# Optimization experiments

Measured on AMD Instinct MI355X. Metric: run time of the kernel, lower is better.

Reference implementation:

```python
import jax, jax.numpy as jnp
import numpy as np

N_NODES = 50000
N_EDGES = 800000
F_IN = 128
F_HID = 128
N_CLS = 1
E_TR = 100000
E_TE = 20000


def setup_inputs() -> dict:
    key = jax.random.key(0)
    ks = jax.random.split(key, 16)
    inp = {
        'x': jax.random.normal(ks[0], (N_NODES, F_IN), dtype=jnp.float32),
        'edge_index': jax.random.randint(ks[1], (2, N_EDGES), 0, N_NODES, dtype=jnp.int32),
        'pos_edges_train': jax.random.randint(ks[2], (2, E_TR), 0, N_NODES, dtype=jnp.int32),
        'neg_edges_train': jax.random.randint(ks[3], (2, E_TR), 0, N_NODES, dtype=jnp.int32),
        'pos_edges_test': jax.random.randint(ks[4], (2, E_TE), 0, N_NODES, dtype=jnp.int32),
        'neg_edges_test': jax.random.randint(ks[5], (2, E_TE), 0, N_NODES, dtype=jnp.int32),
    }
    s = 0.05
    inp['W0'] = jax.random.normal(ks[6], (F_IN, F_HID), dtype=jnp.float32) * s
    inp['b0'] = jnp.zeros((F_HID,), dtype=jnp.float32)
    inp['W1'] = jax.random.normal(ks[7], (F_HID, F_HID), dtype=jnp.float32) * s
    inp['b1'] = jnp.zeros((F_HID,), dtype=jnp.float32)
    inp['W2'] = jax.random.normal(ks[8], (F_HID, F_HID), dtype=jnp.float32) * s
    inp['b2'] = jnp.zeros((F_HID,), dtype=jnp.float32)
    inp['W3'] = jax.random.normal(ks[9], (F_HID, F_HID), dtype=jnp.float32) * s
    inp['b3'] = jnp.zeros((F_HID,), dtype=jnp.float32)
    inp['Wl1'] = jax.random.normal(ks[10], (2 * F_HID, F_HID), dtype=jnp.float32) * s
    inp['bl1'] = jnp.zeros((F_HID,), dtype=jnp.float32)
    inp['Wl2'] = jax.random.normal(ks[11], (F_HID, N_CLS), dtype=jnp.float32) * s
    inp['bl2'] = jnp.zeros((N_CLS,), dtype=jnp.float32)
    return inp


def _gcn_conv(h, W, b, src, dst, dis):
    # PyG GCNConv: out = D^{-1/2}(A+I)D^{-1/2} (h W) + b, with self loops folded in analytically
    hw = h @ W                                           # [N, F]
    msg = hw[src] * dis[src][:, None]                    # [E, F]
    agg = jax.ops.segment_sum(msg, dst, num_segments=N_NODES)
    return agg * dis[:, None] + hw * (dis ** 2)[:, None] + b


def _edge_feats(x, e):
    return jnp.concatenate([x[e[0]], x[e[1]]], axis=1)


def reference(x, edge_index, pos_edges_train, neg_edges_train, pos_edges_test, neg_edges_test,
              W0, b0, W1, b1, W2, b2, W3, b3, Wl1, bl1, Wl2, bl2):
    src, dst = edge_index[0], edge_index[1]
    # degree with self loop (+1), symmetric normalization
    deg = jax.ops.segment_sum(jnp.ones((src.shape[0],), jnp.float32), dst, num_segments=N_NODES) + 1.0
    dis = deg ** -0.5

    h = jax.nn.relu(_gcn_conv(x, W0, b0, src, dst, dis))
    h = jax.nn.relu(_gcn_conv(h, W1, b1, src, dst, dis))
    h = jax.nn.relu(_gcn_conv(h, W2, b2, src, dst, dis))
    h = _gcn_conv(h, W3, b3, src, dst, dis)

    x_train = jnp.concatenate([_edge_feats(h, pos_edges_train), _edge_feats(h, neg_edges_train)], axis=0)
    x_test = jnp.concatenate([_edge_feats(h, pos_edges_test), _edge_feats(h, neg_edges_test)], axis=0)
    n_train = x_train.shape[0]
    z = jnp.concatenate([x_train, x_test], axis=0)
    z = jax.nn.relu(z @ Wl1 + bl1)
    z = (z @ Wl2 + bl2).squeeze(1)
    return (z[:n_train], z[n_train:])
```

## Files before the change

### kernel.cpp

```cpp
#include <hip/hip_runtime.h>
#include <math.h>

#define NN 50000
#define NE 800000
#define FD 128
#define SCAN_B 196


__global__ __launch_bounds__(256) void k_zero_int(int* __restrict__ p, int n) {
    int i = blockIdx.x * 256 + threadIdx.x;
    if (i < n) p[i] = 0;
}

__global__ __launch_bounds__(256) void k_count(const int* __restrict__ dst, int* __restrict__ deg) {
    int e = blockIdx.x * 256 + threadIdx.x;
    if (e < NE) atomicAdd(&deg[dst[e]], 1);
}


__global__ __launch_bounds__(256) void k_scan1(const int* __restrict__ deg,
                                               int* __restrict__ partial,
                                               int* __restrict__ bsum,
                                               float* __restrict__ dis) {
    __shared__ int wsum[4];
    const int t = threadIdx.x, lane = t & 63, wid = t >> 6;
    const int i = blockIdx.x * 256 + t;
    int v = (i < NN) ? deg[i] : 0;
    int sc = v;
#pragma unroll
    for (int d = 1; d < 64; d <<= 1) {
        int o = __shfl_up(sc, d, 64);
        if (lane >= d) sc += o;
    }
    if (lane == 63) wsum[wid] = sc;
    __syncthreads();
    int pre = 0;
    for (int w = 0; w < wid; ++w) pre += wsum[w];
    if (i < NN) {
        partial[i] = pre + sc - v;
        dis[i] = (float)(1.0 / sqrt((double)(v + 1)));
    }
    if (t == 255) bsum[blockIdx.x] = pre + sc;
}


__global__ __launch_bounds__(256) void k_scan2(int* __restrict__ bsum) {
    __shared__ int wsum[4];
    const int t = threadIdx.x, lane = t & 63, wid = t >> 6;
    int v = (t < SCAN_B) ? bsum[t] : 0;
    int sc = v;
#pragma unroll
    for (int d = 1; d < 64; d <<= 1) {
        int o = __shfl_up(sc, d, 64);
        if (lane >= d) sc += o;
    }
    if (lane == 63) wsum[wid] = sc;
    __syncthreads();
    int pre = 0;
    for (int w = 0; w < wid; ++w) pre += wsum[w];
    if (t < SCAN_B) bsum[t] = pre + sc - v;
}


__global__ __launch_bounds__(256) void k_scan3(const int* __restrict__ partial,
                                               const int* __restrict__ bsum,
                                               int* __restrict__ offs,
                                               int* __restrict__ cursor) {
    const int i = blockIdx.x * 256 + threadIdx.x;
    if (i < NN) {
        int o = partial[i] + bsum[blockIdx.x];
        offs[i] = o;
        cursor[i] = o;
    }
    if (i == 0) offs[NN] = NE;
}


__global__ __launch_bounds__(256) void k_fill(const int* __restrict__ src, const int* __restrict__ dst,
                                              int* __restrict__ cursor, int* __restrict__ srcs_sorted) {
    int e = blockIdx.x * 256 + threadIdx.x;
    if (e < NE) {
        int d = dst[e];
        int p = atomicAdd(&cursor[d], 1);
        srcs_sorted[p] = src[e];
    }
}


template <bool SCALE>
__global__ __launch_bounds__(256) void k_gemm(const float* __restrict__ A,
                                              const float* __restrict__ W,
                                              const float* __restrict__ dis,
                                              float* __restrict__ C, int nrows) {
    __shared__ float As[64][128];
    const int t = threadIdx.x;
    const int row0 = blockIdx.x * 64;

    for (int idx = t; idx < 64 * 32; idx += 256) {
        int r = idx >> 5, c = idx & 31;
        float4 v = make_float4(0.f, 0.f, 0.f, 0.f);
        if (row0 + r < nrows)
            v = reinterpret_cast<const float4*>(A)[(size_t)(row0 + r) * 32 + c];
        reinterpret_cast<float4*>(&As[r][0])[c] = v;
    }
    __syncthreads();

    const int cg = t & 31;
    const int eg = t >> 5;
    float acc[8][4] = {{0.f}};

    const float4* W4 = reinterpret_cast<const float4*>(W);
    const float4* As4 = reinterpret_cast<const float4*>(As);

    for (int k4 = 0; k4 < 32; ++k4) {
        float4 w0 = W4[(k4 * 4 + 0) * 32 + cg];
        float4 w1 = W4[(k4 * 4 + 1) * 32 + cg];
        float4 w2 = W4[(k4 * 4 + 2) * 32 + cg];
        float4 w3 = W4[(k4 * 4 + 3) * 32 + cg];
#pragma unroll
        for (int i = 0; i < 8; ++i) {
            float4 a = As4[(eg * 8 + i) * 32 + k4];
            acc[i][0] += a.x * w0.x + a.y * w1.x + a.z * w2.x + a.w * w3.x;
            acc[i][1] += a.x * w0.y + a.y * w1.y + a.z * w2.y + a.w * w3.y;
            acc[i][2] += a.x * w0.z + a.y * w1.z + a.z * w2.z + a.w * w3.z;
            acc[i][3] += a.x * w0.w + a.y * w1.w + a.z * w2.w + a.w * w3.w;
        }
    }

#pragma unroll
    for (int i = 0; i < 8; ++i) {
        int r = row0 + eg * 8 + i;
        if (r < nrows) {
            float d = SCALE ? dis[r] : 1.0f;
            float4 o = make_float4(acc[i][0] * d, acc[i][1] * d, acc[i][2] * d, acc[i][3] * d);
            reinterpret_cast<float4*>(C)[(size_t)r * 32 + cg] = o;
        }
    }
}


template <bool RELU>
__global__ __launch_bounds__(256) void k_gather(const float* __restrict__ hws,
                                                const float* __restrict__ dis,
                                                const float* __restrict__ b,
                                                const int* __restrict__ offs,
                                                const int* __restrict__ srcs,
                                                float* __restrict__ out) {
    const int t = threadIdx.x;
    const int f4 = t & 31;
    const int node = blockIdx.x * 8 + (t >> 5);
    if (node >= NN) return;

    const float4* H4 = reinterpret_cast<const float4*>(hws);
    float4 acc = H4[(size_t)node * 32 + f4];
    const int e0 = offs[node], e1 = offs[node + 1];
    int e = e0;
    for (; e + 4 <= e1; e += 4) {
        int s0 = srcs[e + 0], s1 = srcs[e + 1], s2 = srcs[e + 2], s3 = srcs[e + 3];
        float4 v0 = H4[(size_t)s0 * 32 + f4];
        float4 v1 = H4[(size_t)s1 * 32 + f4];
        float4 v2 = H4[(size_t)s2 * 32 + f4];
        float4 v3 = H4[(size_t)s3 * 32 + f4];
        acc.x += v0.x + v1.x + v2.x + v3.x;
        acc.y += v0.y + v1.y + v2.y + v3.y;
        acc.z += v0.z + v1.z + v2.z + v3.z;
        acc.w += v0.w + v1.w + v2.w + v3.w;
    }
    for (; e < e1; ++e) {
        int s = srcs[e];
        float4 v = H4[(size_t)s * 32 + f4];
        acc.x += v.x; acc.y += v.y; acc.z += v.z; acc.w += v.w;
    }
    float d = dis[node];
    float4 bb = reinterpret_cast<const float4*>(b)[f4];
    float4 o;
    o.x = acc.x * d + bb.x;
    o.y = acc.y * d + bb.y;
    o.z = acc.z * d + bb.z;
    o.w = acc.w * d + bb.w;
    if (RELU) {
        o.x = fmaxf(o.x, 0.f); o.y = fmaxf(o.y, 0.f);
        o.z = fmaxf(o.z, 0.f); o.w = fmaxf(o.w, 0.f);
    }
    reinterpret_cast<float4*>(out)[(size_t)node * 32 + f4] = o;
}


__global__ __launch_bounds__(256) void k_edge_score(const float* __restrict__ U,
                                                    const float* __restrict__ V,
                                                    const int* __restrict__ eA,
                                                    const int* __restrict__ eB,
                                                    const float* __restrict__ bl1,
                                                    const float* __restrict__ Wl2,
                                                    const float* __restrict__ bl2,
                                                    float* __restrict__ out, int nedges) {
    const int t = threadIdx.x;
    const int f4 = t & 31;
    const int e = blockIdx.x * 8 + (t >> 5);
    if (e >= nedges) return;

    int a = eA[e], bn = eB[e];
    float4 u = reinterpret_cast<const float4*>(U)[(size_t)a * 32 + f4];
    float4 v = reinterpret_cast<const float4*>(V)[(size_t)bn * 32 + f4];
    float4 bb = reinterpret_cast<const float4*>(bl1)[f4];
    float4 w2 = reinterpret_cast<const float4*>(Wl2)[f4];

    float s = fmaxf(u.x + v.x + bb.x, 0.f) * w2.x
            + fmaxf(u.y + v.y + bb.y, 0.f) * w2.y
            + fmaxf(u.z + v.z + bb.z, 0.f) * w2.z
            + fmaxf(u.w + v.w + bb.w, 0.f) * w2.w;
#pragma unroll
    for (int m = 16; m >= 1; m >>= 1) s += __shfl_xor(s, m, 64);
    if (f4 == 0) out[e] = s + bl2[0];
}


extern "C" void kernel_launch(void* const* d_in, const int* in_sizes, int n_in,
                              void* d_out, int out_size, void* d_ws, size_t ws_size,
                              hipStream_t stream) {
    const float* x = (const float*)d_in[0];
    const int* ei = (const int*)d_in[1];
    const int* srcp = ei;
    const int* dstp = ei + NE;

    const int* e_tr_pos = (const int*)d_in[2];
    const int* e_tr_neg = (const int*)d_in[3];
    const int* e_te_pos = (const int*)d_in[4];
    const int* e_te_neg = (const int*)d_in[5];

    const float* W[4] = {(const float*)d_in[6], (const float*)d_in[8],
                         (const float*)d_in[10], (const float*)d_in[12]};
    const float* b[4] = {(const float*)d_in[7], (const float*)d_in[9],
                         (const float*)d_in[11], (const float*)d_in[13]};
    const float* Wl1 = (const float*)d_in[14];
    const float* bl1 = (const float*)d_in[15];
    const float* Wl2 = (const float*)d_in[16];
    const float* bl2 = (const float*)d_in[17];

    float* ws = (float*)d_ws;
    float* dis = ws;
    int* deg = (int*)(ws + 50176);
    int* offs = (int*)(ws + 100352);
    int* cursor = (int*)(ws + 150784);
    int* bsum = (int*)(ws + 200960);
    int* srcs = (int*)(ws + 201216);
    float* B0 = ws + 1001216;
    float* B1 = B0 + 6400000;
    float* B2 = B1 + 6400000;
    int* partial = (int*)B2;

    k_zero_int<<<(NN + 255) / 256, 256, 0, stream>>>(deg, NN);
    k_count<<<(NE + 255) / 256, 256, 0, stream>>>(dstp, deg);
    k_scan1<<<SCAN_B, 256, 0, stream>>>(deg, partial, bsum, dis);
    k_scan2<<<1, 256, 0, stream>>>(bsum);
    k_scan3<<<SCAN_B, 256, 0, stream>>>(partial, bsum, offs, cursor);
    k_fill<<<(NE + 255) / 256, 256, 0, stream>>>(srcp, dstp, cursor, srcs);

    const int gemm_blocks = (NN + 63) / 64;
    const int gath_blocks = (NN + 7) / 8;

    float* hout[4] = {B1, B2, B1, B2};
    const float* hin = x;
    for (int l = 0; l < 4; ++l) {
        k_gemm<true><<<gemm_blocks, 256, 0, stream>>>(hin, W[l], dis, B0, NN);
        if (l < 3)
            k_gather<true><<<gath_blocks, 256, 0, stream>>>(B0, dis, b[l], offs, srcs, hout[l]);
        else
            k_gather<false><<<gath_blocks, 256, 0, stream>>>(B0, dis, b[l], offs, srcs, hout[l]);
        hin = hout[l];
    }

    const float* hfin = B2;
    float* Ubuf = B0;
    float* Vbuf = B1;
    k_gemm<false><<<gemm_blocks, 256, 0, stream>>>(hfin, Wl1, dis, Ubuf, NN);
    k_gemm<false><<<gemm_blocks, 256, 0, stream>>>(hfin, Wl1 + 128 * 128, dis, Vbuf, NN);

    float* out = (float*)d_out;
    k_edge_score<<<(100000 + 7) / 8, 256, 0, stream>>>(Ubuf, Vbuf, e_tr_pos, e_tr_pos + 100000,
                                                       bl1, Wl2, bl2, out, 100000);
    k_edge_score<<<(100000 + 7) / 8, 256, 0, stream>>>(Ubuf, Vbuf, e_tr_neg, e_tr_neg + 100000,
                                                       bl1, Wl2, bl2, out + 100000, 100000);
    k_edge_score<<<(20000 + 7) / 8, 256, 0, stream>>>(Ubuf, Vbuf, e_te_pos, e_te_pos + 20000,
                                                      bl1, Wl2, bl2, out + 200000, 20000);
    k_edge_score<<<(20000 + 7) / 8, 256, 0, stream>>>(Ubuf, Vbuf, e_te_neg, e_te_neg + 20000,
                                                      bl1, Wl2, bl2, out + 220000, 20000);
}
```

Measured before the change: 569.6 us.

## Slice gather by feature chunks, fuse U/V GEMMs and edge-score launches

New measurement: 653.9 us. 1.15x slower.

```diff
diff --git a/kernel.cpp b/kernel.cpp
--- a/kernel.cpp
+++ b/kernel.cpp
@@ -5,6 +5,8 @@
 #define NE 800000
 #define FD 128
 #define SCAN_B 196
+#define NTR 100000
+#define NTE 20000
 
 
 __global__ __launch_bounds__(256) void k_zero_int(int* __restrict__ p, int n) {
@@ -43,7 +45,6 @@
     if (t == 255) bsum[blockIdx.x] = pre + sc;
 }
 
-
 __global__ __launch_bounds__(256) void k_scan2(int* __restrict__ bsum) {
     __shared__ int wsum[4];
     const int t = threadIdx.x, lane = t & 63, wid = t >> 6;
@@ -60,7 +61,6 @@
     for (int w = 0; w < wid; ++w) pre += wsum[w];
     if (t < SCAN_B) bsum[t] = pre + sc - v;
 }
-
 
 __global__ __launch_bounds__(256) void k_scan3(const int* __restrict__ partial,
                                                const int* __restrict__ bsum,
@@ -87,7 +87,6 @@
 }
 
 
-template <bool SCALE>
 __global__ __launch_bounds__(256) void k_gemm(const float* __restrict__ A,
                                               const float* __restrict__ W,
                                               const float* __restrict__ dis,
@@ -131,9 +130,68 @@
     for (int i = 0; i < 8; ++i) {
         int r = row0 + eg * 8 + i;
         if (r < nrows) {
-            float d = SCALE ? dis[r] : 1.0f;
+            float d = dis[r];
             float4 o = make_float4(acc[i][0] * d, acc[i][1] * d, acc[i][2] * d, acc[i][3] * d);
             reinterpret_cast<float4*>(C)[(size_t)r * 32 + cg] = o;
+        }
+    }
+}
+
+
+__global__ __launch_bounds__(256) void k_gemm_uv(const float* __restrict__ A,
+                                                 const float* __restrict__ Wa,
+                                                 const float* __restrict__ Wb,
+                                                 float* __restrict__ U,
+                                                 float* __restrict__ V, int nrows) {
+    __shared__ float As[64][128];
+    const int t = threadIdx.x;
+    const int row0 = blockIdx.x * 64;
+
+    for (int idx = t; idx < 64 * 32; idx += 256) {
+        int r = idx >> 5, c = idx & 31;
+        float4 v = make_float4(0.f, 0.f, 0.f, 0.f);
+        if (row0 + r < nrows)
+            v = reinterpret_cast<const float4*>(A)[(size_t)(row0 + r) * 32 + c];
+        reinterpret_cast<float4*>(&As[r][0])[c] = v;
+    }
+    __syncthreads();
+
+    const int cg = t & 31;
+    const int eg = t >> 5;
+    float accU[8][4] = {{0.f}};
+    float accV[8][4] = {{0.f}};
+
+    const float4* Wa4 = reinterpret_cast<const float4*>(Wa);
+    const float4* Wb4 = reinterpret_cast<const float4*>(Wb);
+    const float4* As4 = reinterpret_cast<const float4*>(As);
+
+    for (int k = 0; k < 128; k += 2) {
+        float4 wa0 = Wa4[(k + 0) * 32 + cg];
+        float4 wa1 = Wa4[(k + 1) * 32 + cg];
+        float4 wb0 = Wb4[(k + 0) * 32 + cg];
+        float4 wb1 = Wb4[(k + 1) * 32 + cg];
+#pragma unroll
+        for (int i = 0; i < 8; ++i) {
+            float2 a = reinterpret_cast<const float2*>(&As[eg * 8 + i][0])[k >> 1];
+            accU[i][0] += a.x * wa0.x + a.y * wa1.x;
+            accU[i][1] += a.x * wa0.y + a.y * wa1.y;
+            accU[i][2] += a.x * wa0.z + a.y * wa1.z;
+            accU[i][3] += a.x * wa0.w + a.y * wa1.w;
+            accV[i][0] += a.x * wb0.x + a.y * wb1.x;
+            accV[i][1] += a.x * wb0.y + a.y * wb1.y;
+            accV[i][2] += a.x * wb0.z + a.y * wb1.z;
+            accV[i][3] += a.x * wb0.w + a.y * wb1.w;
+        }
+    }
+
+#pragma unroll
+    for (int i = 0; i < 8; ++i) {
+        int r = row0 + eg * 8 + i;
+        if (r < nrows) {
+            reinterpret_cast<float4*>(U)[(size_t)r * 32 + cg] =
+                make_float4(accU[i][0], accU[i][1], accU[i][2], accU[i][3]);
+            reinterpret_cast<float4*>(V)[(size_t)r * 32 + cg] =
+                make_float4(accV[i][0], accV[i][1], accV[i][2], accV[i][3]);
         }
     }
 }
@@ -147,9 +205,10 @@
                                                 const int* __restrict__ srcs,
                                                 float* __restrict__ out) {
     const int t = threadIdx.x;
-    const int f4 = t & 31;
-    const int node = blockIdx.x * 8 + (t >> 5);
+    const int slice = blockIdx.x & 7;
+    const int node = (blockIdx.x >> 3) * 64 + (t >> 2);
     if (node >= NN) return;
+    const int f4 = slice * 4 + (t & 3);
 
     const float4* H4 = reinterpret_cast<const float4*>(hws);
     float4 acc = H4[(size_t)node * 32 + f4];
@@ -188,18 +247,25 @@
 
 __global__ __launch_bounds__(256) void k_edge_score(const float* __restrict__ U,
                                                     const float* __restrict__ V,
-                                                    const int* __restrict__ eA,
-                                                    const int* __restrict__ eB,
+                                                    const int* __restrict__ tp,
+                                                    const int* __restrict__ tn,
+                                                    const int* __restrict__ sp,
+                                                    const int* __restrict__ sn,
                                                     const float* __restrict__ bl1,
                                                     const float* __restrict__ Wl2,
                                                     const float* __restrict__ bl2,
-                                                    float* __restrict__ out, int nedges) {
+                                                    float* __restrict__ out) {
     const int t = threadIdx.x;
     const int f4 = t & 31;
     const int e = blockIdx.x * 8 + (t >> 5);
-    if (e >= nedges) return;
-
-    int a = eA[e], bn = eB[e];
+    if (e >= 2 * NTR + 2 * NTE) return;
+
+    int a, bn;
+    if (e < NTR)                { a = tp[e];              bn = tp[e + NTR]; }
+    else if (e < 2 * NTR)       { a = tn[e - NTR];        bn = tn[e]; }
+    else if (e < 2 * NTR + NTE) { a = sp[e - 2 * NTR];    bn = sp[e - 2 * NTR + NTE]; }
+    else                        { a = sn[e - 2 * NTR - NTE]; bn = sn[e - 2 * NTR]; }
+
     float4 u = reinterpret_cast<const float4*>(U)[(size_t)a * 32 + f4];
     float4 v = reinterpret_cast<const float4*>(V)[(size_t)bn * 32 + f4];
     float4 bb = reinterpret_cast<const float4*>(bl1)[f4];
@@ -257,12 +323,12 @@
     k_fill<<<(NE + 255) / 256, 256, 0, stream>>>(srcp, dstp, cursor, srcs);
 
     const int gemm_blocks = (NN + 63) / 64;
-    const int gath_blocks = (NN + 7) / 8;
+    const int gath_blocks = ((NN + 63) / 64) * 8;
 
     float* hout[4] = {B1, B2, B1, B2};
     const float* hin = x;
     for (int l = 0; l < 4; ++l) {
-        k_gemm<true><<<gemm_blocks, 256, 0, stream>>>(hin, W[l], dis, B0, NN);
+        k_gemm<<<gemm_blocks, 256, 0, stream>>>(hin, W[l], dis, B0, NN);
         if (l < 3)
             k_gather<true><<<gath_blocks, 256, 0, stream>>>(B0, dis, b[l], offs, srcs, hout[l]);
         else
@@ -273,16 +339,11 @@
     const float* hfin = B2;
     float* Ubuf = B0;
     float* Vbuf = B1;
-    k_gemm<false><<<gemm_blocks, 256, 0, stream>>>(hfin, Wl1, dis, Ubuf, NN);
-    k_gemm<false><<<gemm_blocks, 256, 0, stream>>>(hfin, Wl1 + 128 * 128, dis, Vbuf, NN);
+    k_gemm_uv<<<gemm_blocks, 256, 0, stream>>>(hfin, Wl1, Wl1 + 128 * 128, Ubuf, Vbuf, NN);
 
     float* out = (float*)d_out;
-    k_edge_score<<<(100000 + 7) / 8, 256, 0, stream>>>(Ubuf, Vbuf, e_tr_pos, e_tr_pos + 100000,
-                                                       bl1, Wl2, bl2, out, 100000);
-    k_edge_score<<<(100000 + 7) / 8, 256, 0, stream>>>(Ubuf, Vbuf, e_tr_neg, e_tr_neg + 100000,
-                                                       bl1, Wl2, bl2, out + 100000, 100000);
-    k_edge_score<<<(20000 + 7) / 8, 256, 0, stream>>>(Ubuf, Vbuf, e_te_pos, e_te_pos + 20000,
-                                                      bl1, Wl2, bl2, out + 200000, 20000);
-    k_edge_score<<<(20000 + 7) / 8, 256, 0, stream>>>(Ubuf, Vbuf, e_te_neg, e_te_neg + 20000,
-                                                      bl1, Wl2, bl2, out + 220000, 20000);
-}
+    const int n_all = 2 * NTR + 2 * NTE;
+    k_edge_score<<<(n_all + 7) / 8, 256, 0, stream>>>(Ubuf, Vbuf,
+                                                      e_tr_pos, e_tr_neg, e_te_pos, e_te_neg,
+                                                      bl1, Wl2, bl2, out);
+}
```
